# Kernel optimization log

Hardware: AMD Instinct MI355X
Metric: run time of the kernel (lower is better)

The kernel has to match this reference:

```python
import jax, jax.numpy as jnp
import numpy as np
from jax.scipy.linalg import cho_solve

N = 4096        # num nodes
D = 256         # in_dim == out_dim
NUM_HOPS = 2
R = 32          # subspace_dim
ETA = 0.5
EPS_SUB = 0.5   # eps in coeff = r / (n * eps^2)
LN_EPS = 1e-5


def setup_inputs() -> dict:
    rng = np.random.default_rng(0)
    K = NUM_HOPS + 1
    # sparse-ish binary adjacency mask with self loops
    mask = (rng.random((N, N)) < 0.002).astype(np.float32)
    mask = np.maximum(mask, np.eye(N, dtype=np.float32))
    deg = mask.sum(axis=1, keepdims=True)
    A = (mask / deg).astype(np.float32)          # row-stochastic propagation
    L = (np.eye(N, dtype=np.float32) - A)        # normalized Laplacian
    H = rng.standard_normal((N, D)).astype(np.float32)
    # orthonormal subspace bases per hop, as in __init__ (QR of randn)
    U = np.stack([np.linalg.qr(rng.standard_normal((D, R)))[0][:, :R] for _ in range(K)]).astype(np.float32)
    lambda_laps = np.full((K,), 0.1, dtype=np.float32)
    hop_weights = np.full((K,), 1.0 / K, dtype=np.float32)
    threshold = np.full((D,), 0.05, dtype=np.float32)
    gamma = np.ones((D,), dtype=np.float32)
    beta = np.zeros((D,), dtype=np.float32)
    return {
        "H": jnp.asarray(H), "A": jnp.asarray(A), "adj_mask": jnp.asarray(mask),
        "L": jnp.asarray(L), "U": jnp.asarray(U),
        "lambda_laps": jnp.asarray(lambda_laps), "hop_weights": jnp.asarray(hop_weights),
        "threshold": jnp.asarray(threshold), "gamma": jnp.asarray(gamma), "beta": jnp.asarray(beta),
    }


def reference(H, A, adj_mask, L, U, lambda_laps, hop_weights, threshold, gamma, beta):
    n, d = H.shape
    r = U.shape[-1]
    # multi-hop propagation
    hops = [H]
    Hk = H
    for _ in range(NUM_HOPS):
        Hk = A @ Hk
        hops.append(Hk)
    w = jax.nn.softmax(hop_weights)
    laps = jax.nn.softplus(lambda_laps)
    coeff = r / (n * EPS_SUB ** 2)
    neg = (1.0 - adj_mask) * -1e9
    I_r = jnp.eye(r, dtype=H.dtype)
    agg = jnp.zeros_like(H)        # accumulates grad_k.T, shape [n, d]
    lap_total = jnp.zeros_like(H)
    for k, H_k in enumerate(hops):
        Uk = U[k]                  # [d, r]
        Zk = Uk.T @ H_k.T          # [r, n]
        M = I_r + coeff * (Zk @ Zk.T)              # [r, r], SPD
        Lc = jnp.linalg.cholesky(M)
        M_inv = cho_solve((Lc, True), I_r)         # cholesky_inverse
        MZ = M_inv @ Zk                            # [r, n]
        scores = Zk.T @ MZ + neg                   # [n, n] masked subspace attention
        alpha = jax.nn.softmax(scores, axis=1)
        grad_k = (Uk @ (MZ @ alpha.T)).T           # [n, d]
        agg = agg + w[k] * grad_k
        lap_total = lap_total + laps[k] * (L @ H_k)
    H_half = H + ETA * agg - ETA * lap_total
    # soft-threshold (proj is None since in_dim == out_dim)
    H_out = jnp.sign(H_half) * jax.nn.relu(jnp.abs(H_half) - threshold[None, :])
    H_out = H_out + H              # residual
    mu = H_out.mean(axis=-1, keepdims=True)
    var = H_out.var(axis=-1, keepdims=True)
    H_out = (H_out - mu) / jnp.sqrt(var + LN_EPS) * gamma + beta
    # orthogonality loss over all (k, l) pairs
    K = U.shape[0]
    orth_loss = jnp.asarray(0.0, dtype=H.dtype)
    for k in range(K):
        for l in range(k, K):
            G = U[k].T @ U[l]
            orth_loss = orth_loss + jnp.sum(((G - I_r) if l == k else G) ** 2)
    lap_smooth = jnp.sum(H_out * (L @ H_out))  # trace(H^T L H)
    return H_out, orth_loss, lap_smooth, jax.lax.stop_gradient(w)
```

## Files before the change

kernel.cpp:

```cpp
#include <hip/hip_runtime.h>
#include <math.h>

#define NN 4096
#define DD 256
#define KK 3
#define RR 32
#define MAXNNZ 128

static constexpr float ETA    = 0.5f;
static constexpr float COEFF  = 0.03125f;
static constexpr float LN_EPSF = 1e-5f;

#define OFF_H1   0
#define OFF_H2   (NN*DD)
#define OFF_H3   (2*NN*DD)
#define OFF_Y    (3*NN*DD)
#define OFF_P    (OFF_Y + KK*NN*RR)
#define OFF_M    (OFF_P + KK*NN*RR)
#define OFF_MINV (OFF_M + KK*RR*RR)
#define OFF_SCAL (OFF_MINV + KK*RR*RR)
#define OFF_NNZ  (OFF_SCAL + 8)
#define OFF_COLS (OFF_NNZ + NN)
#define OFF_VALS (OFF_COLS + NN*MAXNNZ)
#define OFF_PART (OFF_VALS + NN*MAXNNZ)
#define OFF_ORTH (OFF_PART + NN/4)
#define OFF_W    (OFF_ORTH + 8)

__global__ __launch_bounds__(256, 8)
void k_csr_prep(const float* __restrict__ A, int* __restrict__ nnz,
                int* __restrict__ cols, float* __restrict__ vals,
                const float* __restrict__ hw, const float* __restrict__ ll,
                const float* __restrict__ U,
                float* __restrict__ ws, float* __restrict__ out) {
  int b = blockIdx.x;
  int t = threadIdx.x;
  if (b >= NN/2) {
    int p = b - NN/2;
    if (p == 6) {
      if (t == 0) {
        float m = fmaxf(fmaxf(hw[0], hw[1]), hw[2]);
        float e0 = expf(hw[0]-m), e1 = expf(hw[1]-m), e2 = expf(hw[2]-m);
        float s = e0 + e1 + e2;
        float w0 = e0/s, w1 = e1/s, w2 = e2/s;
        ws[OFF_SCAL+0] = w0; ws[OFF_SCAL+1] = w1; ws[OFF_SCAL+2] = w2;
        for (int k = 0; k < KK; ++k) {
          float x = ll[k];
          ws[OFF_SCAL+3+k] = (x > 20.f) ? x : log1pf(expf(x));
        }
        out[NN*DD + 2] = w0; out[NN*DD + 3] = w1; out[NN*DD + 4] = w2;
      }
      for (int idx = t; idx < KK*RR*RR; idx += 256) {
        int rr2 = idx % (RR*RR);
        ws[OFF_M + idx] = ((rr2 / RR) == (rr2 % RR)) ? 1.f : 0.f;
      }
      return;
    }
    int k = (p < 3) ? 0 : ((p < 5) ? 1 : 2);
    int l = (p < 3) ? p : ((p < 5) ? p - 2 : 2);
    int a0 = t >> 5, bb = t & 31;
    float s0 = 0.f, s1 = 0.f, s2 = 0.f, s3 = 0.f;
    for (int dd = 0; dd < DD; ++dd) {
      float ul = U[(size_t)l*DD*RR + dd*RR + bb];
      const float* uk = U + (size_t)k*DD*RR + dd*RR;
      s0 += uk[a0]      * ul;
      s1 += uk[a0 + 8]  * ul;
      s2 += uk[a0 + 16] * ul;
      s3 += uk[a0 + 24] * ul;
    }
    if (k == l && bb == a0)      s0 -= 1.f;
    if (k == l && bb == a0 + 8)  s1 -= 1.f;
    if (k == l && bb == a0 + 16) s2 -= 1.f;
    if (k == l && bb == a0 + 24) s3 -= 1.f;
    float sq = s0*s0 + s1*s1 + s2*s2 + s3*s3;
    #pragma unroll
    for (int o = 32; o > 0; o >>= 1) sq += __shfl_xor(sq, o, 64);
    __shared__ float red[4];
    if ((t & 63) == 0) red[t >> 6] = sq;
    __syncthreads();
    if (t == 0) ws[OFF_ORTH + p] = red[0] + red[1] + red[2] + red[3];
    return;
  }
  int w = t >> 6, lane = t & 63;
  int r = w >> 1, h2 = w & 1;
  int i = b * 2 + r;
  __shared__ int   cbuf[2][2][MAXNNZ];
  __shared__ float vbuf[2][2][MAXNNZ];
  __shared__ int   cnts[4];
  const float4* row4 = (const float4*)(A + (size_t)i * NN);
  float4 vv[8];
  #pragma unroll
  for (int it = 0; it < 8; ++it) vv[it] = row4[h2*512 + it*64 + lane];
  unsigned long long lower = lane ? (~0ull >> (64 - lane)) : 0ull;
  int base = 0;
  #pragma unroll
  for (int it = 0; it < 8; ++it) {
    float4 v = vv[it];
    int jb = (h2*512 + it*64 + lane) * 4;
    unsigned long long mx = __ballot(v.x != 0.f);
    unsigned long long my = __ballot(v.y != 0.f);
    unsigned long long mz = __ballot(v.z != 0.f);
    unsigned long long mw = __ballot(v.w != 0.f);
    int before = __popcll(mx & lower) + __popcll(my & lower)
               + __popcll(mz & lower) + __popcll(mw & lower);
    int p0 = base + before;
    int bx = (mx >> lane) & 1, by = (my >> lane) & 1, bz = (mz >> lane) & 1;
    if (v.x != 0.f && p0 < MAXNNZ)  { cbuf[r][h2][p0] = jb;   vbuf[r][h2][p0] = v.x; }
    int p1 = p0 + bx;
    if (v.y != 0.f && p1 < MAXNNZ)  { cbuf[r][h2][p1] = jb+1; vbuf[r][h2][p1] = v.y; }
    int p2 = p1 + by;
    if (v.z != 0.f && p2 < MAXNNZ)  { cbuf[r][h2][p2] = jb+2; vbuf[r][h2][p2] = v.z; }
    int p3 = p2 + bz;
    if (v.w != 0.f && p3 < MAXNNZ)  { cbuf[r][h2][p3] = jb+3; vbuf[r][h2][p3] = v.w; }
    base += __popcll(mx) + __popcll(my) + __popcll(mz) + __popcll(mw);
  }
  if (lane == 0) cnts[w] = base < MAXNNZ ? base : MAXNNZ;
  __syncthreads();
  int rr = t >> 7, e0 = t & 127;
  int ii = b * 2 + rr;
  int n0 = cnts[rr*2], n1 = cnts[rr*2 + 1];
  int n = n0 + n1; if (n > MAXNNZ) n = MAXNNZ;
  int npad = (n + 7) & ~7;
  for (int e = e0; e < npad; e += 128) {
    int c; float v;
    if (e < n) {
      if (e < n0) { c = cbuf[rr][0][e];      v = vbuf[rr][0][e]; }
      else        { c = cbuf[rr][1][e - n0]; v = vbuf[rr][1][e - n0]; }
    } else { c = ii; v = 0.f; }
    cols[ii*MAXNNZ + e] = c;
    vals[ii*MAXNNZ + e] = v;
  }
  if (e0 == 0) nnz[ii] = n;
}

__device__ __forceinline__ void spmv_quad(const float* __restrict__ X, int row, int lane,
                                          const int* __restrict__ nnz,
                                          const int* __restrict__ cols,
                                          const float* __restrict__ vals,
                                          float4& acc, float4& own) {
  int d4 = lane * 4;
  int n = nnz[row];
  int npad = (n + 7) & ~7;
  const int* ci = cols + row*MAXNNZ;
  const float* vi = vals + row*MAXNNZ;
  for (int e0 = 0; e0 < npad; e0 += 8) {
    int4 c0 = *(const int4*)(ci + e0);
    int4 c1 = *(const int4*)(ci + e0 + 4);
    float4 v0 = *(const float4*)(vi + e0);
    float4 v1 = *(const float4*)(vi + e0 + 4);
    float4 x0 = *(const float4*)(X + (size_t)c0.x*DD + d4);
    float4 x1 = *(const float4*)(X + (size_t)c0.y*DD + d4);
    float4 x2 = *(const float4*)(X + (size_t)c0.z*DD + d4);
    float4 x3 = *(const float4*)(X + (size_t)c0.w*DD + d4);
    float4 x4 = *(const float4*)(X + (size_t)c1.x*DD + d4);
    float4 x5 = *(const float4*)(X + (size_t)c1.y*DD + d4);
    float4 x6 = *(const float4*)(X + (size_t)c1.z*DD + d4);
    float4 x7 = *(const float4*)(X + (size_t)c1.w*DD + d4);
    if (c0.x == row) own = x0;
    if (c0.y == row) own = x1;
    if (c0.z == row) own = x2;
    if (c0.w == row) own = x3;
    if (c1.x == row) own = x4;
    if (c1.y == row) own = x5;
    if (c1.z == row) own = x6;
    if (c1.w == row) own = x7;
    acc.x += v0.x*x0.x + v0.y*x1.x + v0.z*x2.x + v0.w*x3.x + v1.x*x4.x + v1.y*x5.x + v1.z*x6.x + v1.w*x7.x;
    acc.y += v0.x*x0.y + v0.y*x1.y + v0.z*x2.y + v0.w*x3.y + v1.x*x4.y + v1.y*x5.y + v1.z*x6.y + v1.w*x7.y;
    acc.z += v0.x*x0.z + v0.y*x1.z + v0.z*x2.z + v0.w*x3.z + v1.x*x4.z + v1.y*x5.z + v1.z*x6.z + v1.w*x7.z;
    acc.w += v0.x*x0.w + v0.y*x1.w + v0.z*x2.w + v0.w*x3.w + v1.x*x4.w + v1.y*x5.w + v1.z*x6.w + v1.w*x7.w;
  }
}

__global__ void k_spmvy(const float* __restrict__ X, float* __restrict__ Hout,
                        const int* __restrict__ nnz, const int* __restrict__ cols,
                        const float* __restrict__ vals,
                        const float* __restrict__ Uo, float* __restrict__ Yo,
                        const float* __restrict__ Un, float* __restrict__ Yn) {
  int t = threadIdx.x;
  int r = t >> 6, lane = t & 63;
  int row = blockIdx.x * 4 + r;
  int d4 = lane * 4;
  float4 acc = {0.f, 0.f, 0.f, 0.f};
  float4 own = {0.f, 0.f, 0.f, 0.f};
  spmv_quad(X, row, lane, nnz, cols, vals, acc, own);
  *(float4*)(Hout + (size_t)row*DD + d4) = acc;
  if (!Uo && !Un) return;
  __shared__ float Hs[4][2][DD];
  *(float4*)&Hs[r][0][d4] = own;
  *(float4*)&Hs[r][1][d4] = acc;
  __syncthreads();
  int c = lane & 31, h = lane >> 5;
  if (Uo) {
    float part = 0.f;
    #pragma unroll 8
    for (int d = h*128; d < h*128 + 128; ++d) part += Hs[r][0][d] * Uo[d*RR + c];
    part += __shfl_xor(part, 32, 64);
    if (h == 0) Yo[(size_t)row*RR + c] = part;
  }
  if (Un) {
    float part = 0.f;
    #pragma unroll 8
    for (int d = h*128; d < h*128 + 128; ++d) part += Hs[r][1][d] * Un[d*RR + c];
    part += __shfl_xor(part, 32, 64);
    if (h == 0) Yn[(size_t)row*RR + c] = part;
  }
}

__global__ __launch_bounds__(1024) void k_gram(const float* __restrict__ Y, float* __restrict__ M) {
  int k = blockIdx.y;
  __shared__ float Ys[128*RR];
  int t = threadIdx.x;
  const float* Yk = Y + (size_t)k*NN*RR + (size_t)blockIdx.x*128*RR;
  for (int idx = t; idx < 128*RR; idx += 1024) Ys[idx] = Yk[idx];
  __syncthreads();
  int a = t >> 5, b = t & 31;
  float s = 0.f;
  for (int i = 0; i < 128; ++i) s += Ys[i*RR + a] * Ys[i*RR + b];
  atomicAdd(&M[k*RR*RR + a*RR + b], COEFF * s);
}

__global__ __launch_bounds__(256) void k_gj(const float* __restrict__ M, float* __restrict__ Minv,
                                            const float* __restrict__ U, float* __restrict__ W) {
  int k = blockIdx.x;
  int g = blockIdx.y;
  int t = threadIdx.x;
  __shared__ float B[RR][2*RR + 1];
  for (int idx = t; idx < RR*2*RR; idx += 256) {
    int r = idx >> 6, c = idx & 63;
    B[r][c] = (c < RR) ? M[k*RR*RR + r*RR + c] : ((c - RR == r) ? 1.f : 0.f);
  }
  __syncthreads();
  if (t < 64) {
    for (int p = 0; p < RR; ++p) {
      float rd = 1.f / B[p][p];
      float pb = B[p][t] * rd;
      float f[RR];
      #pragma unroll
      for (int r = 0; r < RR; ++r) f[r] = B[r][p];
      B[p][t] = pb;
      #pragma unroll
      for (int r = 0; r < RR; ++r) {
        if (r == p) continue;
        B[r][t] -= f[r] * pb;
      }
    }
  }
  __syncthreads();
  if (g == 0)
    for (int idx = t; idx < RR*RR; idx += 256)
      Minv[k*RR*RR + idx] = B[idx >> 5][RR + (idx & 31)];
  for (int e = 0; e < 8; ++e) {
    int idx = t + e*256;
    int d = g*64 + (idx >> 5), rr2 = idx & 31;
    const float* ud = U + (size_t)k*DD*RR + (size_t)d*RR;
    float s = 0.f;
    #pragma unroll
    for (int a = 0; a < RR; ++a) s += ud[a] * B[a][RR + rr2];
    W[(size_t)k*DD*RR + (size_t)d*RR + rr2] = s;
  }
}

__global__ __launch_bounds__(256) void k_attn(const float* __restrict__ Y, const float* __restrict__ Minv,
                       float* __restrict__ P, const int* __restrict__ nnz,
                       const int* __restrict__ cols, const float* __restrict__ vals,
                       const float* __restrict__ H2, float* __restrict__ H3) {
  int k = blockIdx.y;
  int t = threadIdx.x;
  int w = t >> 6, lane = t & 63;
  if (blockIdx.x >= NN/4) {
    if (k != 0) return;
    int row = (blockIdx.x - NN/4) * 4 + w;
    float4 acc = {0.f, 0.f, 0.f, 0.f};
    float4 own;
    spmv_quad(H2, row, lane, nnz, cols, vals, acc, own);
    *(float4*)(H3 + (size_t)row*DD + lane*4) = acc;
    return;
  }
  int i = blockIdx.x * 4 + w;
  const float* Yk = Y + (size_t)k*NN*RR;
  __shared__ float Mi[RR*RR];
  __shared__ float Yi[4][RR];
  __shared__ float qv[4][RR];
  __shared__ float sc[4][MAXNNZ];
  __shared__ float Yc[4][32][RR + 1];
  for (int idx = t; idx < RR*RR; idx += 256) Mi[idx] = Minv[k*RR*RR + idx];
  if (lane < RR) Yi[w][lane] = Yk[(size_t)i*RR + lane];
  sc[w][lane] = -1e30f; sc[w][lane+64] = -1e30f;
  __syncthreads();
  if (lane < RR) {
    float s = 0.f;
    #pragma unroll 8
    for (int a = 0; a < RR; ++a) s += Mi[a*RR + lane] * Yi[w][a];
    qv[w][lane] = s;
  }
  int g = lane >> 2, a4 = lane & 3;
  const float* qq = &qv[w][8*a4];
  float q0 = qq[0], q1 = qq[1], q2 = qq[2], q3 = qq[3];
  float q4 = qq[4], q5 = qq[5], q6 = qq[6], q7 = qq[7];
  int n = nnz[i], npad = (n + 7) & ~7;
  const int* ci = cols + i*MAXNNZ;
  for (int e0 = 0; e0 < npad; e0 += 16) {
    int e = e0 + g;
    int ee = (e < npad) ? e : 0;
    int col = ci[ee];
    const float4* yr = (const float4*)(Yk + (size_t)col*RR + 8*a4);
    float4 y0 = yr[0], y1 = yr[1];
    if (e < 32) {
      *(float4*)&Yc[w][e][8*a4]     = y0;
      *(float4*)&Yc[w][e][8*a4 + 4] = y1;
    }
    float s = y0.x*q0 + y0.y*q1 + y0.z*q2 + y0.w*q3
            + y1.x*q4 + y1.y*q5 + y1.z*q6 + y1.w*q7;
    s += __shfl_xor(s, 1, 64);
    s += __shfl_xor(s, 2, 64);
    if (a4 == 0 && e < npad) sc[w][e] = (e < n) ? s : -1e30f;
  }
  float s0 = sc[w][lane], s1 = sc[w][lane+64];
  float m = fmaxf(s0, s1);
  #pragma unroll
  for (int o = 32; o > 0; o >>= 1) m = fmaxf(m, __shfl_xor(m, o, 64));
  float e0v = expf(s0 - m), e1v = expf(s1 - m);
  sc[w][lane] = e0v; sc[w][lane+64] = e1v;
  float l = e0v + e1v;
  #pragma unroll
  for (int o = 32; o > 0; o >>= 1) l += __shfl_xor(l, o, 64);
  float linv = 1.f / l;
  int c = lane & 31, h = lane >> 5;
  float acc = 0.f;
  int lim = npad < 32 ? npad : 32;
  for (int e = h; e < lim; e += 2) acc += sc[w][e] * Yc[w][e][c];
  for (int e = 32 + h; e < npad; e += 2) acc += sc[w][e] * Yk[(size_t)ci[e]*RR + c];
  acc += __shfl_xor(acc, 32, 64);
  if (lane < RR) P[(size_t)k*NN*RR + (size_t)i*RR + lane] = acc * linv;
}

__global__ void k_epi(const float* __restrict__ H0, const float* __restrict__ ws,
                      const float* __restrict__ thr,
                      const float* __restrict__ gma, const float* __restrict__ bta,
                      float* __restrict__ out) {
  __shared__ float Us[DD][RR+1];
  __shared__ float Ps[8][KK*RR];
  int t = threadIdx.x;
  int ty = t >> 5, tx = t & 31;
  int row0 = blockIdx.x * 8;
  const float* P    = ws + OFF_P;
  const float* scal = ws + OFF_SCAL;
  const float* W    = ws + OFF_W;
  for (int idx = t; idx < 8*KK*RR; idx += 256) {
    int rl = idx / (KK*RR), kr = idx % (KK*RR);
    int k = kr / RR, rr2 = kr % RR;
    Ps[rl][kr] = P[(size_t)k*NN*RR + (size_t)(row0+rl)*RR + rr2];
  }
  float lp0 = scal[3], lp1 = scal[4], lp2 = scal[5];
  float gacc[8];
  #pragma unroll
  for (int j = 0; j < 8; ++j) gacc[j] = 0.f;
  for (int k = 0; k < KK; ++k) {
    __syncthreads();
    for (int idx = t; idx < DD*RR/4; idx += 256) {
      float4 w4 = *(const float4*)(W + (size_t)k*DD*RR + (size_t)idx*4);
      int d = (idx*4) >> 5, c = (idx*4) & 31;
      Us[d][c] = w4.x; Us[d][c+1] = w4.y; Us[d][c+2] = w4.z; Us[d][c+3] = w4.w;
    }
    __syncthreads();
    float wk = scal[k];
    #pragma unroll
    for (int j = 0; j < 8; ++j) {
      int d = tx + 32*j;
      float s = 0.f;
      #pragma unroll
      for (int rr2 = 0; rr2 < RR; ++rr2) s += Ps[ty][k*RR + rr2] * Us[d][rr2];
      gacc[j] += wk * s;
    }
  }
  int i = row0 + ty;
  const float* H1 = ws + OFF_H1;
  const float* H2 = ws + OFF_H2;
  const float* H3 = ws + OFF_H3;
  float v[8]; float sum = 0.f, sumsq = 0.f;
  #pragma unroll
  for (int j = 0; j < 8; ++j) {
    int d = tx + 32*j;
    size_t idx = (size_t)i*DD + d;
    float h0 = H0[idx], h1 = H1[idx], h2 = H2[idx], h3 = H3[idx];
    float lap = lp0*(h0-h1) + lp1*(h1-h2) + lp2*(h2-h3);
    float hf = h0 + ETA*gacc[j] - ETA*lap;
    float a = fabsf(hf) - thr[d];
    float sft = (a > 0.f) ? copysignf(a, hf) : 0.f;
    float x = sft + h0;
    v[j] = x; sum += x; sumsq += x*x;
  }
  #pragma unroll
  for (int o = 16; o > 0; o >>= 1) {
    sum   += __shfl_xor(sum, o, 32);
    sumsq += __shfl_xor(sumsq, o, 32);
  }
  float mu  = sum * (1.f/DD);
  float var = sumsq * (1.f/DD) - mu*mu;
  float inv = rsqrtf(var + LN_EPSF);
  #pragma unroll
  for (int j = 0; j < 8; ++j) {
    int d = tx + 32*j;
    out[(size_t)i*DD + d] = (v[j] - mu) * inv * gma[d] + bta[d];
  }
}

__global__ void k_lapsm(const float* __restrict__ Hout, const int* __restrict__ nnz,
                        const int* __restrict__ cols, const float* __restrict__ vals,
                        float* __restrict__ partial) {
  int t = threadIdx.x;
  int row = blockIdx.x * 4 + (t >> 6);
  int d4 = (t & 63) * 4;
  int n = nnz[row];
  int npad = (n + 7) & ~7;
  const int* ci = cols + row*MAXNNZ;
  const float* vi = vals + row*MAXNNZ;
  float4 acc = {0.f, 0.f, 0.f, 0.f};
  for (int e0 = 0; e0 < npad; e0 += 8) {
    int4 c0 = *(const int4*)(ci + e0);
    int4 c1 = *(const int4*)(ci + e0 + 4);
    float4 v0 = *(const float4*)(vi + e0);
    float4 v1 = *(const float4*)(vi + e0 + 4);
    float4 x0 = *(const float4*)(Hout + (size_t)c0.x*DD + d4);
    float4 x1 = *(const float4*)(Hout + (size_t)c0.y*DD + d4);
    float4 x2 = *(const float4*)(Hout + (size_t)c0.z*DD + d4);
    float4 x3 = *(const float4*)(Hout + (size_t)c0.w*DD + d4);
    float4 x4 = *(const float4*)(Hout + (size_t)c1.x*DD + d4);
    float4 x5 = *(const float4*)(Hout + (size_t)c1.y*DD + d4);
    float4 x6 = *(const float4*)(Hout + (size_t)c1.z*DD + d4);
    float4 x7 = *(const float4*)(Hout + (size_t)c1.w*DD + d4);
    acc.x += v0.x*x0.x + v0.y*x1.x + v0.z*x2.x + v0.w*x3.x + v1.x*x4.x + v1.y*x5.x + v1.z*x6.x + v1.w*x7.x;
    acc.y += v0.x*x0.y + v0.y*x1.y + v0.z*x2.y + v0.w*x3.y + v1.x*x4.y + v1.y*x5.y + v1.z*x6.y + v1.w*x7.y;
    acc.z += v0.x*x0.z + v0.y*x1.z + v0.z*x2.z + v0.w*x3.z + v1.x*x4.z + v1.y*x5.z + v1.z*x6.z + v1.w*x7.z;
    acc.w += v0.x*x0.w + v0.y*x1.w + v0.z*x2.w + v0.w*x3.w + v1.x*x4.w + v1.y*x5.w + v1.z*x6.w + v1.w*x7.w;
  }
  float4 h = *(const float4*)(Hout + (size_t)row*DD + d4);
  float part = h.x*(h.x-acc.x) + h.y*(h.y-acc.y) + h.z*(h.z-acc.z) + h.w*(h.w-acc.w);
  #pragma unroll
  for (int o = 32; o > 0; o >>= 1) part += __shfl_xor(part, o, 64);
  __shared__ float red[4];
  if ((t & 63) == 0) red[t >> 6] = part;
  __syncthreads();
  if (t == 0) partial[blockIdx.x] = red[0] + red[1] + red[2] + red[3];
}

__global__ void k_red(const float* __restrict__ ws, float* __restrict__ out) {
  const float* partial = ws + OFF_PART;
  int t = threadIdx.x;
  float4 p = *(const float4*)(partial + t*4);
  float s = p.x + p.y + p.z + p.w;
  #pragma unroll
  for (int o = 32; o > 0; o >>= 1) s += __shfl_xor(s, o, 64);
  __shared__ float red[4];
  if ((t & 63) == 0) red[t >> 6] = s;
  __syncthreads();
  if (t == 0) {
    out[1] = red[0] + red[1] + red[2] + red[3];
    const float* op = ws + OFF_ORTH;
    out[0] = op[0] + op[1] + op[2] + op[3] + op[4] + op[5];
  }
}

extern "C" void kernel_launch(void* const* d_in, const int* in_sizes, int n_in,
                              void* d_out, int out_size, void* d_ws, size_t ws_size,
                              hipStream_t stream) {
  const float* H   = (const float*)d_in[0];
  const float* A   = (const float*)d_in[1];
  const float* U   = (const float*)d_in[4];
  const float* ll  = (const float*)d_in[5];
  const float* hw  = (const float*)d_in[6];
  const float* thr = (const float*)d_in[7];
  const float* gma = (const float*)d_in[8];
  const float* bta = (const float*)d_in[9];
  float* out = (float*)d_out;
  float* ws  = (float*)d_ws;
  int* nnz   = (int*)(ws + OFF_NNZ);
  int* cols  = (int*)(ws + OFF_COLS);
  float* vals = ws + OFF_VALS;
  float* Y = ws + OFF_Y;

  k_csr_prep<<<NN/2 + 7, 256, 0, stream>>>(A, nnz, cols, vals, hw, ll, U, ws, out);
  k_spmvy<<<NN/4, 256, 0, stream>>>(H, ws + OFF_H1, nnz, cols, vals,
                                    U, Y, U + (size_t)DD*RR, Y + (size_t)NN*RR);
  k_spmvy<<<NN/4, 256, 0, stream>>>(ws + OFF_H1, ws + OFF_H2, nnz, cols, vals,
                                    nullptr, nullptr, U + (size_t)2*DD*RR, Y + (size_t)2*NN*RR);
  dim3 g32(NN/128, KK);
  k_gram<<<g32, 1024, 0, stream>>>(Y, ws + OFF_M);
  dim3 ggj(KK, 4);
  k_gj<<<ggj, 256, 0, stream>>>(ws + OFF_M, ws + OFF_MINV, U, ws + OFF_W);
  dim3 gattn(NN/4 + NN/4, KK);
  k_attn<<<gattn, 256, 0, stream>>>(Y, ws + OFF_MINV, ws + OFF_P, nnz, cols, vals,
                                    ws + OFF_H2, ws + OFF_H3);
  k_epi<<<NN/8, 256, 0, stream>>>(H, ws, thr, gma, bta, out);
  k_lapsm<<<NN/4, 256, 0, stream>>>(out, nnz, cols, vals, ws + OFF_PART);
  k_red<<<1, 256, 0, stream>>>(ws, out + NN*DD);
}
```

Baseline: 288.5 us.

## Fuse first-hop SpMV and Y projections into CSR prep kernel

The CSR extraction kernel now keeps each row's compressed columns and values in shared memory and immediately computes the first propagation hop A@H for its two rows. It also computes the hop-0 and hop-1 subspace projections (H·U0, H1·U1). This removes one kernel launch and the re-read of the CSR arrays from global memory. In exchange, half the waves sit idle during the SpMV, the shared-memory footprint grows, and the occupancy hint drops from 8 to 4 blocks, which may slow the bandwidth-bound scan of the dense A.

```diff
diff --git a/kernel.cpp b/kernel.cpp
--- a/kernel.cpp
+++ b/kernel.cpp
@@ -26,12 +26,13 @@
 #define OFF_ORTH (OFF_PART + NN/4)
 #define OFF_W    (OFF_ORTH + 8)
 
-__global__ __launch_bounds__(256, 8)
+__global__ __launch_bounds__(256, 4)
 void k_csr_prep(const float* __restrict__ A, int* __restrict__ nnz,
                 int* __restrict__ cols, float* __restrict__ vals,
                 const float* __restrict__ hw, const float* __restrict__ ll,
                 const float* __restrict__ U,
-                float* __restrict__ ws, float* __restrict__ out) {
+                float* __restrict__ ws, float* __restrict__ out,
+                const float* __restrict__ H) {
   int b = blockIdx.x;
   int t = threadIdx.x;
   if (b >= NN/2) {
@@ -85,7 +86,11 @@
   int i = b * 2 + r;
   __shared__ int   cbuf[2][2][MAXNNZ];
   __shared__ float vbuf[2][2][MAXNNZ];
+  __shared__ int   csr_c[2][MAXNNZ];
+  __shared__ float csr_v[2][MAXNNZ];
   __shared__ int   cnts[4];
+  __shared__ int   nnzs[2];
+  __shared__ float Hs[2][2][DD];
   const float4* row4 = (const float4*)(A + (size_t)i * NN);
   float4 vv[8];
   #pragma unroll
@@ -115,21 +120,78 @@
   }
   if (lane == 0) cnts[w] = base < MAXNNZ ? base : MAXNNZ;
   __syncthreads();
-  int rr = t >> 7, e0 = t & 127;
-  int ii = b * 2 + rr;
-  int n0 = cnts[rr*2], n1 = cnts[rr*2 + 1];
-  int n = n0 + n1; if (n > MAXNNZ) n = MAXNNZ;
-  int npad = (n + 7) & ~7;
-  for (int e = e0; e < npad; e += 128) {
-    int c; float v;
-    if (e < n) {
-      if (e < n0) { c = cbuf[rr][0][e];      v = vbuf[rr][0][e]; }
-      else        { c = cbuf[rr][1][e - n0]; v = vbuf[rr][1][e - n0]; }
-    } else { c = ii; v = 0.f; }
-    cols[ii*MAXNNZ + e] = c;
-    vals[ii*MAXNNZ + e] = v;
-  }
-  if (e0 == 0) nnz[ii] = n;
+  {
+    int rr = t >> 7, e0 = t & 127;
+    int ii = b * 2 + rr;
+    int n0 = cnts[rr*2], n1 = cnts[rr*2 + 1];
+    int n = n0 + n1; if (n > MAXNNZ) n = MAXNNZ;
+    int npad = (n + 7) & ~7;
+    for (int e = e0; e < npad; e += 128) {
+      int c; float v;
+      if (e < n) {
+        if (e < n0) { c = cbuf[rr][0][e];      v = vbuf[rr][0][e]; }
+        else        { c = cbuf[rr][1][e - n0]; v = vbuf[rr][1][e - n0]; }
+      } else { c = ii; v = 0.f; }
+      cols[ii*MAXNNZ + e] = c;
+      vals[ii*MAXNNZ + e] = v;
+      csr_c[rr][e] = c;
+      csr_v[rr][e] = v;
+    }
+    if (e0 == 0) { nnz[ii] = n; nnzs[rr] = n; }
+  }
+  __syncthreads();
+  float* H1 = ws + OFF_H1;
+  if ((w & 1) == 0) {
+    int rI = w >> 1;
+    int row = b * 2 + rI;
+    int d4 = lane * 4;
+    int n2 = nnzs[rI], npad2 = (n2 + 7) & ~7;
+    float4 acc = {0.f, 0.f, 0.f, 0.f};
+    float4 own = {0.f, 0.f, 0.f, 0.f};
+    for (int e0i = 0; e0i < npad2; e0i += 8) {
+      int4 c0 = *(const int4*)&csr_c[rI][e0i];
+      int4 c1 = *(const int4*)&csr_c[rI][e0i + 4];
+      float4 v0 = *(const float4*)&csr_v[rI][e0i];
+      float4 v1 = *(const float4*)&csr_v[rI][e0i + 4];
+      float4 x0 = *(const float4*)(H + (size_t)c0.x*DD + d4);
+      float4 x1 = *(const float4*)(H + (size_t)c0.y*DD + d4);
+      float4 x2 = *(const float4*)(H + (size_t)c0.z*DD + d4);
+      float4 x3 = *(const float4*)(H + (size_t)c0.w*DD + d4);
+      float4 x4 = *(const float4*)(H + (size_t)c1.x*DD + d4);
+      float4 x5 = *(const float4*)(H + (size_t)c1.y*DD + d4);
+      float4 x6 = *(const float4*)(H + (size_t)c1.z*DD + d4);
+      float4 x7 = *(const float4*)(H + (size_t)c1.w*DD + d4);
+      if (c0.x == row) own = x0;
+      if (c0.y == row) own = x1;
+      if (c0.z == row) own = x2;
+      if (c0.w == row) own = x3;
+      if (c1.x == row) own = x4;
+      if (c1.y == row) own = x5;
+      if (c1.z == row) own = x6;
+      if (c1.w == row) own = x7;
+      acc.x += v0.x*x0.x + v0.y*x1.x + v0.z*x2.x + v0.w*x3.x + v1.x*x4.x + v1.y*x5.x + v1.z*x6.x + v1.w*x7.x;
+      acc.y += v0.x*x0.y + v0.y*x1.y + v0.z*x2.y + v0.w*x3.y + v1.x*x4.y + v1.y*x5.y + v1.z*x6.y + v1.w*x7.y;
+      acc.z += v0.x*x0.z + v0.y*x1.z + v0.z*x2.z + v0.w*x3.z + v1.x*x4.z + v1.y*x5.z + v1.z*x6.z + v1.w*x7.z;
+      acc.w += v0.x*x0.w + v0.y*x1.w + v0.z*x2.w + v0.w*x3.w + v1.x*x4.w + v1.y*x5.w + v1.z*x6.w + v1.w*x7.w;
+    }
+    *(float4*)(H1 + (size_t)row*DD + d4) = acc;
+    *(float4*)&Hs[rI][0][d4] = own;
+    *(float4*)&Hs[rI][1][d4] = acc;
+  }
+  __syncthreads();
+  {
+    int rI = w >> 1;
+    int row = b * 2 + rI;
+    int useAcc = w & 1;
+    const float* Up = U + (size_t)useAcc*DD*RR;
+    float* Yp = ws + OFF_Y + (size_t)useAcc*NN*RR;
+    int c = lane & 31, h = lane >> 5;
+    float part = 0.f;
+    #pragma unroll 8
+    for (int d = h*128; d < h*128 + 128; ++d) part += Hs[rI][useAcc][d] * Up[d*RR + c];
+    part += __shfl_xor(part, 32, 64);
+    if (h == 0) Yp[(size_t)row*RR + c] = part;
+  }
 }
 
 __device__ __forceinline__ void spmv_quad(const float* __restrict__ X, int row, int lane,
@@ -478,9 +540,7 @@
   float* vals = ws + OFF_VALS;
   float* Y = ws + OFF_Y;
 
-  k_csr_prep<<<NN/2 + 7, 256, 0, stream>>>(A, nnz, cols, vals, hw, ll, U, ws, out);
-  k_spmvy<<<NN/4, 256, 0, stream>>>(H, ws + OFF_H1, nnz, cols, vals,
-                                    U, Y, U + (size_t)DD*RR, Y + (size_t)NN*RR);
+  k_csr_prep<<<NN/2 + 7, 256, 0, stream>>>(A, nnz, cols, vals, hw, ll, U, ws, out, H);
   k_spmvy<<<NN/4, 256, 0, stream>>>(ws + OFF_H1, ws + OFF_H2, nnz, cols, vals,
                                     nullptr, nullptr, U + (size_t)2*DD*RR, Y + (size_t)2*NN*RR);
   dim3 g32(NN/128, KK);
```

New measurement: 280.2 us (median of 2 runs). -2.9%, faster.
